# Optimization experiments

Measured on AMD Instinct MI355X. Metric: run time of the kernel, lower is better.

Reference implementation:

```python
import jax, jax.numpy as jnp
import numpy as np

B, N, C, H = 2, 2048, 1024, 16
D = C // H  # head_dim = 64


def setup_inputs() -> dict:
    key = jax.random.key(0)
    ks = jax.random.split(key, 5)
    s = 1.0 / np.sqrt(C)
    return {
        "q": jax.random.normal(ks[0], (B, N, C), dtype=jnp.float32),
        "W_qkv": jax.random.normal(ks[1], (C, 3 * C), dtype=jnp.float32) * s,
        "b_qkv": jnp.zeros((3 * C,), dtype=jnp.float32),
        "W_proj": jax.random.normal(ks[2], (C, C), dtype=jnp.float32) * s,
        "b_proj": jnp.zeros((C,), dtype=jnp.float32),
    }


def reference(q, W_qkv, b_qkv, W_proj, b_proj):
    # Self-attention: k = v = q. Full 3C projection (as in the torch code).
    qkv = q @ W_qkv + b_qkv  # [B, N, 3C]
    qh = qkv[:, :, :C].reshape(B, N, H, D)
    kh = qkv[:, :, C:2 * C].reshape(B, N, H, D)
    vh = qkv[:, :, 2 * C:].reshape(B, N, H, D)
    scale = D ** -0.5
    # [B, H, N, N] attention logits
    attn = jnp.einsum("bnhd,bmhd->bhnm", qh, kh) * scale
    attn = jax.nn.softmax(attn, axis=-1)
    out = jnp.einsum("bhnm,bmhd->bnhd", attn, vh).reshape(B, N, C)
    return out @ W_proj + b_proj
```

## Files before the change

### kernel.cpp

```cpp
#include <hip/hip_runtime.h>
#include <stdint.h>

typedef __bf16 bf16_t;
typedef __bf16 bf16x8 __attribute__((ext_vector_type(8)));
typedef __bf16 bf16x4 __attribute__((ext_vector_type(4)));
typedef float f32x4 __attribute__((ext_vector_type(4)));

#define L2E 1.44269504088896340736f
#define QSCALE (0.125f * L2E)

__device__ __forceinline__ void gload16(const bf16_t* g, bf16_t* l) {
  __builtin_amdgcn_global_load_lds(
      (const __attribute__((address_space(1))) void*)g,
      (__attribute__((address_space(3))) void*)l, 16, 0, 0);
}

__device__ __forceinline__ float fexp2(float x) {
  float r;
  asm("v_exp_f32 %0, %1" : "=v"(r) : "v"(x));
  return r;
}

__global__ __launch_bounds__(256) void prep_kernel(const float* __restrict__ qin,
                                                   bf16_t* __restrict__ qbf,
                                                   const float* __restrict__ wqkv,
                                                   bf16_t* __restrict__ wqkv_t,
                                                   const float* __restrict__ wproj,
                                                   bf16_t* __restrict__ wproj_t) {
  __shared__ float tile[64][65];
  const int bid = blockIdx.x, t = threadIdx.x;
  if (bid < 4096) {
    int i = bid * 256 + t;
    float4 v = reinterpret_cast<const float4*>(qin)[i];
    bf16x4 o;
    o[0] = (bf16_t)v.x; o[1] = (bf16_t)v.y; o[2] = (bf16_t)v.z; o[3] = (bf16_t)v.w;
    reinterpret_cast<bf16x4*>(qbf)[i] = o;
    return;
  }
  const float* in; bf16_t* out; int N, bx, by;
  if (bid < 4864) {
    int bb = bid - 4096; in = wqkv; out = wqkv_t; N = 3072; bx = bb % 48; by = bb / 48;
  } else {
    int bb = bid - 4864; in = wproj; out = wproj_t; N = 1024; bx = bb % 16; by = bb / 16;
  }
  const int K = 1024;
  int k0 = by * 64, n0 = bx * 64;
  int r = t >> 4, c4 = (t & 15) * 4;
#pragma unroll
  for (int rr = 0; rr < 4; rr++) {
    int row = r + rr * 16;
    float4 v = *reinterpret_cast<const float4*>(&in[(size_t)(k0 + row) * N + n0 + c4]);
    tile[row][c4 + 0] = v.x; tile[row][c4 + 1] = v.y;
    tile[row][c4 + 2] = v.z; tile[row][c4 + 3] = v.w;
  }
  __syncthreads();
#pragma unroll
  for (int rr = 0; rr < 4; rr++) {
    int nr = r + rr * 16;
    bf16x4 o;
#pragma unroll
    for (int i = 0; i < 4; i++) o[i] = (bf16_t)tile[c4 + i][nr];
    *reinterpret_cast<bf16x4*>(&out[(size_t)(n0 + nr) * K + k0 + c4]) = o;
  }
}

template <int MODE, int BM>
__global__ __launch_bounds__(256) void gemm_kernel(const bf16_t* __restrict__ A,
                                                   const bf16_t* __restrict__ Bt,
                                                   const float* __restrict__ bias,
                                                   void* __restrict__ out,
                                                   bf16_t* __restrict__ vT,
                                                   int K, int gm, int gn, int ldo) {
  constexpr int ACH = BM / 8;
  constexpr int NCH = ACH + 16;
  constexpr int CPW = NCH / 4;
  constexpr int IR = BM / 32;
  constexpr int SMEM = 17408;
  __shared__ __align__(16) bf16_t smem[SMEM];
  bf16_t* At = smem;
  bf16_t* Bts = smem + BM * 64;
  const int t = threadIdx.x, lane = t & 63, w = t >> 6;
  const int g = lane >> 4, q = lane & 15;
  const int bid = blockIdx.x, x = bid & 7, r = bid >> 3;
  const int qm = gm >> 2, qn = gn >> 1;
  const int lm = r % qm, ln = r / qm;
  const int m0 = ((x & 3) * qm + lm) * BM, n0 = ((x >> 2) * qn + ln) * 128;
  const int wm = (w >> 1) * (BM / 2), wn = (w & 1) * 64;

  const bf16_t* srcp[CPW]; int dsto[CPW];
#pragma unroll
  for (int i = 0; i < CPW; i++) {
    int cI = i * 4 + w;
    bool isA = cI < ACH;
    int row = (isA ? cI : cI - ACH) * 8 + (lane >> 3);
    int p = (lane & 7) ^ (row & 7);
    srcp[i] = (isA ? A + (size_t)(m0 + row) * K : Bt + (size_t)(n0 + row) * K) + p * 8;
    dsto[i] = (isA ? cI * 512 : BM * 64 + (cI - ACH) * 512);
  }

  f32x4 acc[IR][4];
#pragma unroll
  for (int i = 0; i < IR; i++)
#pragma unroll
    for (int j = 0; j < 4; j++) acc[i][j] = (f32x4){0.f, 0.f, 0.f, 0.f};

  for (int k0 = 0; k0 < K; k0 += 64) {
    __syncthreads();
#pragma unroll
    for (int i = 0; i < CPW; i++) gload16(srcp[i] + k0, &smem[dsto[i]]);
    __syncthreads();
#pragma unroll
    for (int dc = 0; dc < 2; dc++) {
      bf16x8 am[IR], bn[4];
#pragma unroll
      for (int i = 0; i < IR; i++) {
        int ra = wm + 16 * i + q;
        am[i] = *reinterpret_cast<const bf16x8*>(&At[ra * 64 + ((dc * 32 + g * 8) ^ ((ra & 7) * 8))]);
      }
#pragma unroll
      for (int j = 0; j < 4; j++) {
        int rb = wn + 16 * j + q;
        bn[j] = *reinterpret_cast<const bf16x8*>(&Bts[rb * 64 + ((dc * 32 + g * 8) ^ ((rb & 7) * 8))]);
      }
#pragma unroll
      for (int i = 0; i < IR; i++)
#pragma unroll
        for (int j = 0; j < 4; j++)
          acc[i][j] = __builtin_amdgcn_mfma_f32_16x16x32_bf16(am[i], bn[j], acc[i][j], 0, 0, 0);
    }
  }

  if (n0 >= 2048) {
    __syncthreads();
    bf16_t* TT = smem;
#pragma unroll
    for (int i = 0; i < IR; i++)
#pragma unroll
      for (int j = 0; j < 4; j++)
#pragma unroll
        for (int rr = 0; rr < 4; rr++) {
          int ch = wn + 16 * j + q;
          int tok = wm + 16 * i + 4 * g + rr;
          float v = acc[i][j][rr] + bias[n0 + ch];
          TT[ch * 136 + (((tok >> 3) ^ (ch & 7)) * 8) + (tok & 7)] = (bf16_t)v;
        }
    __syncthreads();
    const int bb = m0 >> 11;
    const int t0 = m0 & 2047;
#pragma unroll
    for (int it = 0; it < 8; it++) {
      int ch = it * 16 + w * 4 + (lane >> 4);
      int ck = lane & 15;
      uint4 val = *reinterpret_cast<const uint4*>(&TT[ch * 136 + ((ck ^ (ch & 7)) * 8)]);
      int vch = (n0 - 2048) + ch;
      bf16_t* dst = vT + ((size_t)(bb * 16 + (vch >> 6)) * 64 + (vch & 63)) * 2048 + t0 + ck * 8;
      *reinterpret_cast<uint4*>(dst) = val;
    }
  } else {
    const float sc = (n0 < 1024) ? QSCALE : 1.0f;
    __syncthreads();
    bf16_t* TT = smem;
#pragma unroll
    for (int i = 0; i < IR; i++)
#pragma unroll
      for (int j = 0; j < 4; j++)
#pragma unroll
        for (int rr = 0; rr < 4; rr++) {
          int ch = wn + 16 * j + q;
          int tok = wm + 16 * i + 4 * g + rr;
          float v = (acc[i][j][rr] + bias[n0 + ch]) * sc;
          TT[tok * 136 + (((ch >> 3) ^ (tok & 7)) * 8) + (ch & 7)] = (bf16_t)v;
        }
    __syncthreads();
#pragma unroll
    for (int it = 0; it < 8; it++) {
      int tok = it * 16 + (t >> 4);
      int gr = t & 15;
      uint4 val = *reinterpret_cast<const uint4*>(&TT[tok * 136 + ((gr ^ (tok & 7)) * 8)]);
      bf16_t* dst = (bf16_t*)out + (size_t)(m0 + tok) * ldo + n0 + gr * 8;
      *reinterpret_cast<uint4*>(dst) = val;
    }
  }
}

__global__ __launch_bounds__(512) void gemm_proj(const bf16_t* __restrict__ A,
                                                 const bf16_t* __restrict__ Bt,
                                                 const float* __restrict__ bias,
                                                 float* __restrict__ out) {
  __shared__ __align__(16) bf16_t smem[33280];
  const int K = 1024;
  const int t = threadIdx.x, lane = t & 63, w = t >> 6;
  const int g = lane >> 4, q = lane & 15;
  const int kg = w >> 2, lw = w & 3;
  const int bid = blockIdx.x, x = bid & 7, r = bid >> 3;
  const int lm = r % 8, ln = r / 8;
  const int m0 = ((x & 3) * 8 + lm) * 128, n0 = ((x >> 2) * 4 + ln) * 128;
  const int wm = (lw >> 1) * 64, wn = (lw & 1) * 64;
  bf16_t* At = smem + kg * 16384;
  bf16_t* Bts = smem + kg * 16384 + 8192;

  const bf16_t* srcp[8]; int dsto[8];
#pragma unroll
  for (int i = 0; i < 8; i++) {
    int cI = i * 4 + lw;
    bool isA = cI < 16;
    int row = (isA ? cI : cI - 16) * 8 + (lane >> 3);
    int p = (lane & 7) ^ (row & 7);
    srcp[i] = (isA ? A + (size_t)(m0 + row) * K : Bt + (size_t)(n0 + row) * K)
              + kg * 512 + p * 8;
    dsto[i] = kg * 16384 + (isA ? cI * 512 : 8192 + (cI - 16) * 512);
  }

  f32x4 acc[4][4];
#pragma unroll
  for (int i = 0; i < 4; i++)
#pragma unroll
    for (int j = 0; j < 4; j++) acc[i][j] = (f32x4){0.f, 0.f, 0.f, 0.f};

  for (int k0 = 0; k0 < 512; k0 += 64) {
    __syncthreads();
#pragma unroll
    for (int i = 0; i < 8; i++) gload16(srcp[i] + k0, &smem[dsto[i]]);
    __syncthreads();
#pragma unroll
    for (int dc = 0; dc < 2; dc++) {
      bf16x8 am[4], bn[4];
#pragma unroll
      for (int i = 0; i < 4; i++) {
        int ra = wm + 16 * i + q;
        am[i] = *reinterpret_cast<const bf16x8*>(&At[ra * 64 + ((dc * 32 + g * 8) ^ ((ra & 7) * 8))]);
      }
#pragma unroll
      for (int j = 0; j < 4; j++) {
        int rb = wn + 16 * j + q;
        bn[j] = *reinterpret_cast<const bf16x8*>(&Bts[rb * 64 + ((dc * 32 + g * 8) ^ ((rb & 7) * 8))]);
      }
#pragma unroll
      for (int i = 0; i < 4; i++)
#pragma unroll
        for (int j = 0; j < 4; j++)
          acc[i][j] = __builtin_amdgcn_mfma_f32_16x16x32_bf16(am[i], bn[j], acc[i][j], 0, 0, 0);
    }
  }

  __syncthreads();
  float* red = (float*)smem;
  if (kg == 1) {
#pragma unroll
    for (int i = 0; i < 4; i++)
#pragma unroll
      for (int j = 0; j < 4; j++)
#pragma unroll
        for (int rr = 0; rr < 4; rr++)
          red[(wm + 16 * i + 4 * g + rr) * 130 + wn + 16 * j + q] = acc[i][j][rr];
  }
  __syncthreads();
  if (kg == 0) {
#pragma unroll
    for (int i = 0; i < 4; i++)
#pragma unroll
      for (int j = 0; j < 4; j++)
#pragma unroll
        for (int rr = 0; rr < 4; rr++) {
          int row = wm + 16 * i + 4 * g + rr;
          int col = wn + 16 * j + q;
          out[(size_t)(m0 + row) * 1024 + n0 + col] =
              acc[i][j][rr] + red[row * 130 + col] + bias[n0 + col];
        }
  }
}

__global__ __launch_bounds__(256) void attn_kernel(const bf16_t* __restrict__ qk,
                                                   const bf16_t* __restrict__ vT,
                                                   bf16_t* __restrict__ aout) {
  __shared__ __align__(16) bf16_t sK[2][4096];
  __shared__ __align__(16) bf16_t sV[2][4096];
  __shared__ __align__(16) bf16_t sP[4][1024];

  const int t = threadIdx.x, lane = t & 63, w = t >> 6;
  const int g = lane >> 4, q = lane & 15;
  const int bid = blockIdx.x, xr = bid >> 3;
  const int bh = (bid & 7) * 4 + (xr >> 5);
  const int b = bh >> 4, h = bh & 15;
  const int q0 = (xr & 31) * 64 + w * 16;
  const bf16_t* qk_b = qk + (size_t)b * 2048 * 2048;
  const bf16_t* vT_h = vT + (size_t)bh * 64 * 2048;
  bf16_t* Pw = sP[w];

  const bf16_t* srcK[2]; const bf16_t* srcV[2]; int dsto[2];
#pragma unroll
  for (int i = 0; i < 2; i++) {
    int gI = (w * 2 + i) * 64 + lane;
    int row = gI >> 3, p = (gI & 7) ^ (row & 7);
    srcK[i] = qk_b + (size_t)row * 2048 + 1024 + h * 64 + p * 8;
    srcV[i] = vT_h + (size_t)row * 2048 + p * 8;
    dsto[i] = (w * 2 + i) * 512;
  }

  bf16x8 bq[2];
  {
    const bf16_t* qr = qk_b + (size_t)(q0 + q) * 2048 + h * 64;
    bq[0] = *reinterpret_cast<const bf16x8*>(qr + g * 8);
    bq[1] = *reinterpret_cast<const bf16x8*>(qr + 32 + g * 8);
  }

  bf16x8 ones;
#pragma unroll
  for (int i = 0; i < 8; i++) ones[i] = (bf16_t)1.0f;

  f32x4 oacc[4];
#pragma unroll
  for (int c = 0; c < 4; c++) oacc[c] = (f32x4){0.f, 0.f, 0.f, 0.f};
  f32x4 lacc = (f32x4){0.f, 0.f, 0.f, 0.f};

#pragma unroll
  for (int i = 0; i < 2; i++) {
    gload16(srcK[i], &sK[0][dsto[i]]);
    gload16(srcV[i], &sV[0][dsto[i]]);
  }
  __syncthreads();

  for (int tt = 0; tt < 32; tt++) {
    const int cur = tt & 1;
    if (tt + 1 < 32) {
      size_t koffK = (size_t)(tt + 1) * 64 * 2048;
      size_t koffV = (size_t)(tt + 1) * 64;
#pragma unroll
      for (int i = 0; i < 2; i++) {
        gload16(srcK[i] + koffK, &sK[cur ^ 1][dsto[i]]);
        gload16(srcV[i] + koffV, &sV[cur ^ 1][dsto[i]]);
      }
    }

    const bf16_t* Kc = sK[cur];
    f32x4 s[4];
#pragma unroll
    for (int c = 0; c < 4; c++) {
      int row = 16 * c + q, sw = (q & 7) * 8;
      bf16x8 ka0 = *reinterpret_cast<const bf16x8*>(&Kc[row * 64 + ((g * 8) ^ sw)]);
      bf16x8 ka1 = *reinterpret_cast<const bf16x8*>(&Kc[row * 64 + ((32 + g * 8) ^ sw)]);
      f32x4 z = (f32x4){0.f, 0.f, 0.f, 0.f};
      z = __builtin_amdgcn_mfma_f32_16x16x32_bf16(ka0, bq[0], z, 0, 0, 0);
      z = __builtin_amdgcn_mfma_f32_16x16x32_bf16(ka1, bq[1], z, 0, 0, 0);
      s[c] = z;
    }

#pragma unroll
    for (int c = 0; c < 4; c++) {
      bf16x4 pk;
#pragma unroll
      for (int rr = 0; rr < 4; rr++) pk[rr] = (bf16_t)fexp2(s[c][rr]);
      *reinterpret_cast<bf16x4*>(
          &Pw[q * 64 + (((2 * c + (g >> 1)) ^ (q & 7)) * 8) + (g & 1) * 4]) = pk;
    }

    const bf16_t* Vc = sV[cur];
#pragma unroll
    for (int kc = 0; kc < 2; kc++) {
      bf16x8 pb = *reinterpret_cast<const bf16x8*>(
          &Pw[q * 64 + (((kc * 4 + g) ^ (q & 7)) * 8)]);
      lacc = __builtin_amdgcn_mfma_f32_16x16x32_bf16(ones, pb, lacc, 0, 0, 0);
#pragma unroll
      for (int c = 0; c < 4; c++) {
        int row = 16 * c + q;
        bf16x8 va = *reinterpret_cast<const bf16x8*>(
            &Vc[row * 64 + (((kc * 4 + g) ^ (q & 7)) * 8)]);
        oacc[c] = __builtin_amdgcn_mfma_f32_16x16x32_bf16(va, pb, oacc[c], 0, 0, 0);
      }
    }

    __syncthreads();
  }

  float inv = 1.0f / lacc[0];
  bf16_t* orow = aout + (size_t)(b * 2048 + q0 + q) * 1024 + h * 64;
#pragma unroll
  for (int c = 0; c < 4; c++) {
    bf16x4 ov;
#pragma unroll
    for (int rr = 0; rr < 4; rr++) ov[rr] = (bf16_t)(oacc[c][rr] * inv);
    *reinterpret_cast<bf16x4*>(orow + c * 16 + g * 4) = ov;
  }
}

extern "C" void kernel_launch(void* const* d_in, const int* in_sizes, int n_in,
                              void* d_out, int out_size, void* d_ws, size_t ws_size,
                              hipStream_t stream) {
  const float* q     = (const float*)d_in[0];
  const float* Wqkv  = (const float*)d_in[1];
  const float* bqkv  = (const float*)d_in[2];
  const float* Wproj = (const float*)d_in[3];
  const float* bproj = (const float*)d_in[4];
  float* out = (float*)d_out;

  char* ws = (char*)d_ws;
  bf16_t* q_bf    = (bf16_t*)(ws);
  bf16_t* wqkv_t  = (bf16_t*)(ws + 8388608);
  bf16_t* wproj_t = (bf16_t*)(ws + 14680064);
  bf16_t* qk      = (bf16_t*)(ws + 16777216);
  bf16_t* vT      = (bf16_t*)(ws + 33554432);
  bf16_t* aout    = q_bf;

  prep_kernel<<<5120, 256, 0, stream>>>(q, q_bf, Wqkv, wqkv_t, Wproj, wproj_t);
  gemm_kernel<0, 128><<<768, 256, 0, stream>>>(q_bf, wqkv_t, bqkv, qk, vT, 1024, 32, 24, 2048);
  attn_kernel<<<1024, 256, 0, stream>>>(qk, vT, aout);
  gemm_proj<<<256, 512, 0, stream>>>(aout, wproj_t, bproj, out);
}
```

Baseline: 129.8 us.

## Load K and V tiles directly from global memory, dropping LDS staging

Removes the double-buffered LDS staging of K and V tiles, along with the per-iteration block barrier. Each wave now reads its K and V fragments straight from global memory into registers for the MFMAs. This avoids LDS traffic and synchronisation, but every wave (four per block) independently refetches the same K/V data through the caches. Global-load latency is also exposed inside the loop with no explicit prefetch.

```diff
diff --git a/kernel.cpp b/kernel.cpp
--- a/kernel.cpp
+++ b/kernel.cpp
@@ -273,8 +273,6 @@
 __global__ __launch_bounds__(256) void attn_kernel(const bf16_t* __restrict__ qk,
                                                    const bf16_t* __restrict__ vT,
                                                    bf16_t* __restrict__ aout) {
-  __shared__ __align__(16) bf16_t sK[2][4096];
-  __shared__ __align__(16) bf16_t sV[2][4096];
   __shared__ __align__(16) bf16_t sP[4][1024];
 
   const int t = threadIdx.x, lane = t & 63, w = t >> 6;
@@ -287,16 +285,6 @@
   const bf16_t* vT_h = vT + (size_t)bh * 64 * 2048;
   bf16_t* Pw = sP[w];
 
-  const bf16_t* srcK[2]; const bf16_t* srcV[2]; int dsto[2];
-#pragma unroll
-  for (int i = 0; i < 2; i++) {
-    int gI = (w * 2 + i) * 64 + lane;
-    int row = gI >> 3, p = (gI & 7) ^ (row & 7);
-    srcK[i] = qk_b + (size_t)row * 2048 + 1024 + h * 64 + p * 8;
-    srcV[i] = vT_h + (size_t)row * 2048 + p * 8;
-    dsto[i] = (w * 2 + i) * 512;
-  }
-
   bf16x8 bq[2];
   {
     const bf16_t* qr = qk_b + (size_t)(q0 + q) * 2048 + h * 64;
@@ -304,6 +292,13 @@
     bq[1] = *reinterpret_cast<const bf16x8*>(qr + 32 + g * 8);
   }
 
+  const bf16_t* kp[4]; const bf16_t* vp[4];
+#pragma unroll
+  for (int c = 0; c < 4; c++) {
+    kp[c] = qk_b + (size_t)(16 * c + q) * 2048 + 1024 + h * 64 + g * 8;
+    vp[c] = vT_h + (size_t)(16 * c + q) * 2048 + g * 8;
+  }
+
   bf16x8 ones;
 #pragma unroll
   for (int i = 0; i < 8; i++) ones[i] = (bf16_t)1.0f;
@@ -313,36 +308,15 @@
   for (int c = 0; c < 4; c++) oacc[c] = (f32x4){0.f, 0.f, 0.f, 0.f};
   f32x4 lacc = (f32x4){0.f, 0.f, 0.f, 0.f};
 
-#pragma unroll
-  for (int i = 0; i < 2; i++) {
-    gload16(srcK[i], &sK[0][dsto[i]]);
-    gload16(srcV[i], &sV[0][dsto[i]]);
-  }
-  __syncthreads();
-
   for (int tt = 0; tt < 32; tt++) {
-    const int cur = tt & 1;
-    if (tt + 1 < 32) {
-      size_t koffK = (size_t)(tt + 1) * 64 * 2048;
-      size_t koffV = (size_t)(tt + 1) * 64;
-#pragma unroll
-      for (int i = 0; i < 2; i++) {
-        gload16(srcK[i] + koffK, &sK[cur ^ 1][dsto[i]]);
-        gload16(srcV[i] + koffV, &sV[cur ^ 1][dsto[i]]);
-      }
-    }
-
-    const bf16_t* Kc = sK[cur];
     f32x4 s[4];
 #pragma unroll
     for (int c = 0; c < 4; c++) {
-      int row = 16 * c + q, sw = (q & 7) * 8;
-      bf16x8 ka0 = *reinterpret_cast<const bf16x8*>(&Kc[row * 64 + ((g * 8) ^ sw)]);
-      bf16x8 ka1 = *reinterpret_cast<const bf16x8*>(&Kc[row * 64 + ((32 + g * 8) ^ sw)]);
+      bf16x8 ka0 = *reinterpret_cast<const bf16x8*>(kp[c]);
+      bf16x8 ka1 = *reinterpret_cast<const bf16x8*>(kp[c] + 32);
       f32x4 z = (f32x4){0.f, 0.f, 0.f, 0.f};
       z = __builtin_amdgcn_mfma_f32_16x16x32_bf16(ka0, bq[0], z, 0, 0, 0);
-      z = __builtin_amdgcn_mfma_f32_16x16x32_bf16(ka1, bq[1], z, 0, 0, 0);
-      s[c] = z;
+      s[c] = __builtin_amdgcn_mfma_f32_16x16x32_bf16(ka1, bq[1], z, 0, 0, 0);
     }
 
 #pragma unroll
@@ -354,7 +328,6 @@
           &Pw[q * 64 + (((2 * c + (g >> 1)) ^ (q & 7)) * 8) + (g & 1) * 4]) = pk;
     }
 
-    const bf16_t* Vc = sV[cur];
 #pragma unroll
     for (int kc = 0; kc < 2; kc++) {
       bf16x8 pb = *reinterpret_cast<const bf16x8*>(
@@ -362,14 +335,16 @@
       lacc = __builtin_amdgcn_mfma_f32_16x16x32_bf16(ones, pb, lacc, 0, 0, 0);
 #pragma unroll
       for (int c = 0; c < 4; c++) {
-        int row = 16 * c + q;
-        bf16x8 va = *reinterpret_cast<const bf16x8*>(
-            &Vc[row * 64 + (((kc * 4 + g) ^ (q & 7)) * 8)]);
+        bf16x8 va = *reinterpret_cast<const bf16x8*>(vp[c] + kc * 32);
         oacc[c] = __builtin_amdgcn_mfma_f32_16x16x32_bf16(va, pb, oacc[c], 0, 0, 0);
       }
     }
 
-    __syncthreads();
+#pragma unroll
+    for (int c = 0; c < 4; c++) {
+      kp[c] += (size_t)64 * 2048;
+      vp[c] += 64;
+    }
   }
 
   float inv = 1.0f / lacc[0];
```

Result: slower. 300.5 us (+131.4%).
